# Kernel optimization log

Hardware: AMD Instinct MI355X
Metric: run time of the kernel (lower is better)

The kernel has to match this reference:

```python
import math
import jax, jax.numpy as jnp
import numpy as np

N = 100000
E_RAND = 800000
IN_F, HID, OUT_F, HEADS = 128, 64, 64, 4
NOISE_SCALE = 1.0 * math.sqrt(2.0 * math.log(1.25 / 0.05))  # dp_rate=1, eps=1, del=0.05


def setup_inputs() -> dict:
    key = jax.random.key(0)
    ks = jax.random.split(key, 12)
    x = jax.random.normal(ks[0], (N, IN_F), dtype=jnp.float32)
    src_r = jax.random.randint(ks[1], (E_RAND,), 0, N, dtype=jnp.int32)
    dst_r = jax.random.randint(ks[2], (E_RAND,), 0, N, dtype=jnp.int32)
    loops = jnp.arange(N, dtype=jnp.int32)  # add_self_loop
    src = jnp.concatenate([src_r, loops])
    dst = jnp.concatenate([dst_r, loops])
    # layer 0: GATConv(in=128, out=64, heads=4)
    s0 = 1.0 / math.sqrt(IN_F)
    W0 = jax.random.normal(ks[3], (IN_F, HEADS * HID), dtype=jnp.float32) * s0
    al0 = jax.random.normal(ks[4], (HEADS, HID), dtype=jnp.float32) * 0.1
    ar0 = jax.random.normal(ks[5], (HEADS, HID), dtype=jnp.float32) * 0.1
    b0 = jnp.zeros((HEADS * HID,), dtype=jnp.float32)
    # layer 1: GATConv(in=256, out=64, heads=1)
    s1 = 1.0 / math.sqrt(HEADS * HID)
    W1 = jax.random.normal(ks[6], (HEADS * HID, OUT_F), dtype=jnp.float32) * s1
    al1 = jax.random.normal(ks[7], (1, OUT_F), dtype=jnp.float32) * 0.1
    ar1 = jax.random.normal(ks[8], (1, OUT_F), dtype=jnp.float32) * 0.1
    b1 = jnp.zeros((OUT_F,), dtype=jnp.float32)
    # DP gaussian noise added after first GAT layer (torch.normal(0,1,x.shape))
    noise = jax.random.normal(ks[9], (N, HEADS * HID), dtype=jnp.float32)
    return {"x": x, "src": src, "dst": dst, "W0": W0, "al0": al0, "ar0": ar0,
            "b0": b0, "W1": W1, "al1": al1, "ar1": ar1, "b1": b1, "noise": noise}


def gat_conv(x, src, dst, W, al, ar, b, apply_act):
    """DGL GATConv: per-edge attention, edge softmax over dst, scatter-sum."""
    H, D = al.shape
    h = (x @ W).reshape(-1, H, D)                      # [N,H,D]
    el = jnp.sum(h * al, axis=-1)                      # [N,H]
    er = jnp.sum(h * ar, axis=-1)                      # [N,H]
    e = jax.nn.leaky_relu(el[src] + er[dst], 0.2)      # [E,H]
    emax = jax.ops.segment_max(e, dst, num_segments=N) # [N,H]
    a = jnp.exp(e - emax[dst])
    denom = jax.ops.segment_sum(a, dst, num_segments=N)
    alpha = a / denom[dst]                             # [E,H] edge softmax
    msg = h[src] * alpha[:, :, None]                   # [E,H,D]
    out = jax.ops.segment_sum(msg, dst, num_segments=N) + b.reshape(1, H, D)
    if apply_act:
        out = jax.nn.leaky_relu(out, 0.01)             # F.leaky_relu default slope
    return out.reshape(-1, H * D)                      # flatten(1)


def reference(x, src, dst, W0, al0, ar0, b0, W1, al1, ar1, b1, noise):
    h = gat_conv(x, src, dst, W0, al0, ar0, b0, apply_act=True)   # [N, 256]
    h = h + NOISE_SCALE * noise                                   # DP noise after layer 0
    out = gat_conv(h, src, dst, W1, al1, ar1, b1, apply_act=False)  # [N, 64]
    return out
```

## Files before the change

kernel.cpp:

```cpp
#include <hip/hip_runtime.h>
#include <hip/hip_bf16.h>
#include <math.h>

#define IN_F 128
#define HID 64
#define HEADS 4
#define HD0 (HEADS * HID)
#define OUT_F 64
#define NOISE_SCALE 2.5372725354060904f

typedef __bf16 bf16x8 __attribute__((ext_vector_type(8)));
typedef float f32x4 __attribute__((ext_vector_type(4)));
typedef float f4 __attribute__((ext_vector_type(4)));
typedef unsigned int u4 __attribute__((ext_vector_type(4)));

__device__ __forceinline__ float bf2f(unsigned short u) {
    return __uint_as_float(((unsigned)u) << 16);
}
__device__ __forceinline__ unsigned short f2bf(float f) {
    unsigned u = __float_as_uint(f);
    u = u + 0x7fffu + ((u >> 16) & 1u);
    return (unsigned short)(u >> 16);
}

__device__ __forceinline__ void acc8(float* acc, const uint4& u, float wt) {
    acc[0] += wt * __uint_as_float(u.x << 16);
    acc[1] += wt * __uint_as_float(u.x & 0xffff0000u);
    acc[2] += wt * __uint_as_float(u.y << 16);
    acc[3] += wt * __uint_as_float(u.y & 0xffff0000u);
    acc[4] += wt * __uint_as_float(u.z << 16);
    acc[5] += wt * __uint_as_float(u.z & 0xffff0000u);
    acc[6] += wt * __uint_as_float(u.w << 16);
    acc[7] += wt * __uint_as_float(u.w & 0xffff0000u);
}

__device__ __forceinline__ uint4 pack8(const float4& a, const float4& b) {
    uint4 r;
    r.x = (unsigned)f2bf(a.x) | ((unsigned)f2bf(a.y) << 16);
    r.y = (unsigned)f2bf(a.z) | ((unsigned)f2bf(a.w) << 16);
    r.z = (unsigned)f2bf(b.x) | ((unsigned)f2bf(b.y) << 16);
    r.w = (unsigned)f2bf(b.z) | ((unsigned)f2bf(b.w) << 16);
    return r;
}

__global__ __launch_bounds__(256) void prep_kernel(
    int* __restrict__ deg, int N,
    const float* __restrict__ W0, unsigned short* __restrict__ W0t,
    const float* __restrict__ W1, unsigned short* __restrict__ W1t) {
    const int b = blockIdx.x;
    int i = b * 256 + threadIdx.x;
    if (i < N) deg[i] = 0;
    if (b < (IN_F * HD0) / 256) {
        int n = i / IN_F, k = i % IN_F;
        W0t[i] = f2bf(W0[(size_t)k * HD0 + n]);
    } else if (b < (IN_F * HD0) / 256 + (HD0 * OUT_F) / 256) {
        int j = i - IN_F * HD0;
        int n = j / HD0, k = j % HD0;
        W1t[j] = f2bf(W1[(size_t)k * OUT_F + n]);
    }
}

template <int K, int H, int NT, bool CVT>
__global__ __launch_bounds__(256) void gemm_fused_kernel(
    const void* __restrict__ Asrc, const unsigned short* __restrict__ Bt,
    unsigned short* __restrict__ C, const float* __restrict__ al,
    const float* __restrict__ ar, float* __restrict__ el,
    float* __restrict__ er, int M, int NC) {
    constexpr int BSTR = K + 8;
    constexpr int ASTR = 40;
    constexpr int NROWS = 64 * NT;
    constexpr int CSTR = NROWS + 8;
    __shared__ __align__(16) unsigned short Bs[NROWS * BSTR];
    __shared__ __align__(16) unsigned short As[128 * ASTR];
    const unsigned short* Ab = (const unsigned short*)Asrc;
    const float* Af = (const float*)Asrc;
    const int tid = threadIdx.x;
    const int lane = tid & 63, w = tid >> 6;
    const int row0 = blockIdx.y * 128;
    const int n0 = blockIdx.x * NROWS;
    for (int i = tid; i < NROWS * (K / 8); i += 256) {
        int n = i / (K / 8), kc = i % (K / 8);
        *(uint4*)(Bs + n * BSTR + kc * 8) =
            *(const uint4*)(Bt + (size_t)(n0 + n) * K + kc * 8);
    }
    f32x4 acc[2][4 * NT] = {};
    const int q = lane >> 4, c = lane & 15;
    const int r_st = tid >> 1, hh = tid & 1;
    for (int k0 = 0; k0 < K; k0 += 32) {
        int gr = row0 + r_st;
        uint4 av0 = make_uint4(0, 0, 0, 0), av1 = make_uint4(0, 0, 0, 0);
        if (gr < M) {
            if (CVT) {
                const float* xp = Af + (size_t)gr * K + k0 + hh * 16;
                const float4 fa = *(const float4*)xp;
                const float4 fb = *(const float4*)(xp + 4);
                const float4 fc = *(const float4*)(xp + 8);
                const float4 fd = *(const float4*)(xp + 12);
                av0 = pack8(fa, fb);
                av1 = pack8(fc, fd);
            } else {
                const unsigned short* ap = Ab + (size_t)gr * K + k0 + hh * 16;
                av0 = *(const uint4*)(ap);
                av1 = *(const uint4*)(ap + 8);
            }
        }
        __syncthreads();
        *(uint4*)(As + r_st * ASTR + hh * 16) = av0;
        *(uint4*)(As + r_st * ASTR + hh * 16 + 8) = av1;
        __syncthreads();
        bf16x8 af[2], bfr[4 * NT];
        af[0] = *(const bf16x8*)(As + (w * 32 + c) * ASTR + q * 8);
        af[1] = *(const bf16x8*)(As + (w * 32 + 16 + c) * ASTR + q * 8);
#pragma unroll
        for (int nt = 0; nt < 4 * NT; ++nt)
            bfr[nt] = *(const bf16x8*)(Bs + (nt * 16 + c) * BSTR + k0 + q * 8);
#pragma unroll
        for (int mt = 0; mt < 2; ++mt)
#pragma unroll
            for (int nt = 0; nt < 4 * NT; ++nt)
                acc[mt][nt] = __builtin_amdgcn_mfma_f32_16x16x32_bf16(
                    af[mt], bfr[nt], acc[mt][nt], 0, 0, 0);
    }
    float alv[4 * NT], arv[4 * NT];
#pragma unroll
    for (int nt = 0; nt < 4 * NT; ++nt) {
        alv[nt] = al[n0 + nt * 16 + c];
        arv[nt] = ar[n0 + nt * 16 + c];
    }
    __syncthreads();
    unsigned short* Cs = Bs;
    const int headbase = n0 >> 6;
#pragma unroll
    for (int mt = 0; mt < 2; ++mt) {
#pragma unroll
        for (int r = 0; r < 4; ++r) {
            const int row = w * 32 + mt * 16 + q * 4 + r;
            const int grow = row0 + row;
            const bool ok = grow < M;
#pragma unroll
            for (int g = 0; g < NT; ++g) {
                float elp = 0.f, erp = 0.f;
#pragma unroll
                for (int t = 0; t < 4; ++t) {
                    int nt = g * 4 + t;
                    float v = acc[mt][nt][r];
                    elp += v * alv[nt];
                    erp += v * arv[nt];
                    Cs[row * CSTR + nt * 16 + c] = f2bf(v);
                }
#pragma unroll
                for (int o = 8; o > 0; o >>= 1) {
                    elp += __shfl_down(elp, o, 16);
                    erp += __shfl_down(erp, o, 16);
                }
                if (c == 0 && ok) {
                    el[(size_t)grow * H + headbase + g] = elp;
                    er[(size_t)grow * H + headbase + g] = erp;
                }
            }
        }
    }
    __syncthreads();
    constexpr int CPR = NROWS / 8;
    for (int i = tid; i < 128 * CPR; i += 256) {
        int row = i / CPR, ch = i % CPR;
        int grow = row0 + row;
        if (grow < M)
            *(uint4*)(C + (size_t)grow * NC + n0 + ch * 8) =
                *(const uint4*)(Cs + row * CSTR + ch * 8);
    }
}

__global__ __launch_bounds__(256) void degree_kernel(
    const int* __restrict__ dst, int* __restrict__ deg, int E) {
    int e = blockIdx.x * 256 + threadIdx.x;
    if (e < E) atomicAdd(&deg[dst[e]], 1);
}

__global__ __launch_bounds__(256) void scan_block_kernel(
    const int* __restrict__ deg, int* __restrict__ off,
    int* __restrict__ bsum, int N) {
    __shared__ int s[256];
    int i = blockIdx.x * 256 + threadIdx.x;
    int v = (i < N) ? deg[i] : 0;
    s[threadIdx.x] = v;
    __syncthreads();
    for (int d = 1; d < 256; d <<= 1) {
        int t = (threadIdx.x >= d) ? s[threadIdx.x - d] : 0;
        __syncthreads();
        s[threadIdx.x] += t;
        __syncthreads();
    }
    if (i < N) off[i] = s[threadIdx.x] - v;
    if (threadIdx.x == 255) bsum[blockIdx.x] = s[255];
}

__global__ __launch_bounds__(512) void scan_partials_kernel(int* __restrict__ bsum, int nb) {
    __shared__ int s[512];
    int v = (threadIdx.x < nb) ? bsum[threadIdx.x] : 0;
    s[threadIdx.x] = v;
    __syncthreads();
    for (int d = 1; d < 512; d <<= 1) {
        int t = (threadIdx.x >= d) ? s[threadIdx.x - d] : 0;
        __syncthreads();
        s[threadIdx.x] += t;
        __syncthreads();
    }
    if (threadIdx.x < nb) bsum[threadIdx.x] = s[threadIdx.x] - v;
}

__global__ __launch_bounds__(256) void add_offsets_kernel(
    int* __restrict__ off, int* __restrict__ cur,
    const int* __restrict__ bsum, int N, int E) {
    int i = blockIdx.x * 256 + threadIdx.x;
    if (i < N) {
        int v = off[i] + bsum[blockIdx.x];
        off[i] = v;
        cur[i] = v;
    }
    if (i == 0) off[N] = E;
}

__global__ __launch_bounds__(256) void fill_csr_kernel(
    const int* __restrict__ src, const int* __restrict__ dst,
    int* __restrict__ cur, int* __restrict__ csr_src, int E) {
    int e = blockIdx.x * 256 + threadIdx.x;
    if (e >= E) return;
    int d = dst[e];
    int pos = atomicAdd(&cur[d], 1);
    csr_src[pos] = src[e];
}

__global__ __launch_bounds__(256) void agg0_kernel(
    const int* __restrict__ off, const int* __restrict__ csr_src,
    const unsigned short* __restrict__ h,
    const float* __restrict__ el,
    const float* __restrict__ er,
    const float* __restrict__ b0, const float* __restrict__ noise,
    unsigned short* __restrict__ out, int N) {
    int gt = blockIdx.x * 256 + threadIdx.x;
    int n = gt >> 5;
    if (n >= N) return;
    const int lane = gt & 31;
    const int hd = lane >> 3;
    const int f0 = lane << 3;
    const float ern = er[(size_t)n * 4 + hd];
    const int beg = off[n];
    const int last = off[n + 1] - 1;
    float acc[8] = {0.f, 0.f, 0.f, 0.f, 0.f, 0.f, 0.f, 0.f};
    float l = 0.f;
    for (int p = beg; p <= last; p += 4) {
        int i1 = p + 1, i2 = p + 2, i3 = p + 3;
        const bool v1 = i1 <= last, v2 = i2 <= last, v3 = i3 <= last;
        i1 = v1 ? i1 : last;
        i2 = v2 ? i2 : last;
        i3 = v3 ? i3 : last;
        const int s0 = csr_src[p],  s1 = csr_src[i1];
        const int s2 = csr_src[i2], s3 = csr_src[i3];
        float e0 = el[(size_t)s0 * 4 + hd] + ern;
        float e1 = el[(size_t)s1 * 4 + hd] + ern;
        float e2 = el[(size_t)s2 * 4 + hd] + ern;
        float e3 = el[(size_t)s3 * 4 + hd] + ern;
        const uint4 u0 = *(const uint4*)(h + (size_t)s0 * HD0 + f0);
        const uint4 u1 = *(const uint4*)(h + (size_t)s1 * HD0 + f0);
        const uint4 u2 = *(const uint4*)(h + (size_t)s2 * HD0 + f0);
        const uint4 u3 = *(const uint4*)(h + (size_t)s3 * HD0 + f0);
        e0 = e0 > 0.f ? e0 : 0.2f * e0;
        e1 = e1 > 0.f ? e1 : 0.2f * e1;
        e2 = e2 > 0.f ? e2 : 0.2f * e2;
        e3 = e3 > 0.f ? e3 : 0.2f * e3;
        const float w0 = __expf(e0);
        const float w1 = v1 ? __expf(e1) : 0.f;
        const float w2 = v2 ? __expf(e2) : 0.f;
        const float w3 = v3 ? __expf(e3) : 0.f;
        acc8(acc, u0, w0);
        acc8(acc, u1, w1);
        acc8(acc, u2, w2);
        acc8(acc, u3, w3);
        l += (w0 + w1) + (w2 + w3);
    }
    const float rd = 1.f / l;
    const float4 ba = *(const float4*)(b0 + f0);
    const float4 bb = *(const float4*)(b0 + f0 + 4);
    const f4 na = __builtin_nontemporal_load((const f4*)(noise + (size_t)n * HD0 + f0));
    const f4 nb = __builtin_nontemporal_load((const f4*)(noise + (size_t)n * HD0 + f0 + 4));
    float o[8];
    o[0] = acc[0] * rd + ba.x;
    o[1] = acc[1] * rd + ba.y;
    o[2] = acc[2] * rd + ba.z;
    o[3] = acc[3] * rd + ba.w;
    o[4] = acc[4] * rd + bb.x;
    o[5] = acc[5] * rd + bb.y;
    o[6] = acc[6] * rd + bb.z;
    o[7] = acc[7] * rd + bb.w;
#pragma unroll
    for (int j = 0; j < 8; ++j) o[j] = o[j] > 0.f ? o[j] : 0.01f * o[j];
    o[0] += NOISE_SCALE * na.x;
    o[1] += NOISE_SCALE * na.y;
    o[2] += NOISE_SCALE * na.z;
    o[3] += NOISE_SCALE * na.w;
    o[4] += NOISE_SCALE * nb.x;
    o[5] += NOISE_SCALE * nb.y;
    o[6] += NOISE_SCALE * nb.z;
    o[7] += NOISE_SCALE * nb.w;
    uint4 ov;
    ov.x = (unsigned)f2bf(o[0]) | ((unsigned)f2bf(o[1]) << 16);
    ov.y = (unsigned)f2bf(o[2]) | ((unsigned)f2bf(o[3]) << 16);
    ov.z = (unsigned)f2bf(o[4]) | ((unsigned)f2bf(o[5]) << 16);
    ov.w = (unsigned)f2bf(o[6]) | ((unsigned)f2bf(o[7]) << 16);
    *(uint4*)(out + (size_t)n * HD0 + f0) = ov;
}

__global__ __launch_bounds__(256) void agg1_kernel(
    const int* __restrict__ off, const int* __restrict__ csr_src,
    const unsigned short* __restrict__ h,
    const float* __restrict__ el,
    const float* __restrict__ er,
    const float* __restrict__ b1, float* __restrict__ out, int N) {
    int gt = blockIdx.x * 256 + threadIdx.x;
    int n = gt >> 4;
    if (n >= N) return;
    const int lane = gt & 15;
    const int f0 = lane << 2;
    const float ern = er[n];
    const int beg = off[n];
    const int last = off[n + 1] - 1;
    float a0 = 0.f, a1 = 0.f, a2 = 0.f, a3 = 0.f, l = 0.f;
    for (int p = beg; p <= last; p += 4) {
        int i1 = p + 1, i2 = p + 2, i3 = p + 3;
        const bool v1 = i1 <= last, v2 = i2 <= last, v3 = i3 <= last;
        i1 = v1 ? i1 : last;
        i2 = v2 ? i2 : last;
        i3 = v3 ? i3 : last;
        const int s0 = csr_src[p],  s1 = csr_src[i1];
        const int s2 = csr_src[i2], s3 = csr_src[i3];
        float e0 = el[s0] + ern;
        float e1 = el[s1] + ern;
        float e2 = el[s2] + ern;
        float e3 = el[s3] + ern;
        const ushort4 u0 = *(const ushort4*)(h + (size_t)s0 * 64 + f0);
        const ushort4 u1 = *(const ushort4*)(h + (size_t)s1 * 64 + f0);
        const ushort4 u2 = *(const ushort4*)(h + (size_t)s2 * 64 + f0);
        const ushort4 u3 = *(const ushort4*)(h + (size_t)s3 * 64 + f0);
        e0 = e0 > 0.f ? e0 : 0.2f * e0;
        e1 = e1 > 0.f ? e1 : 0.2f * e1;
        e2 = e2 > 0.f ? e2 : 0.2f * e2;
        e3 = e3 > 0.f ? e3 : 0.2f * e3;
        const float w0 = __expf(e0);
        const float w1 = v1 ? __expf(e1) : 0.f;
        const float w2 = v2 ? __expf(e2) : 0.f;
        const float w3 = v3 ? __expf(e3) : 0.f;
        a0 += w0 * bf2f(u0.x) + w1 * bf2f(u1.x) + w2 * bf2f(u2.x) + w3 * bf2f(u3.x);
        a1 += w0 * bf2f(u0.y) + w1 * bf2f(u1.y) + w2 * bf2f(u2.y) + w3 * bf2f(u3.y);
        a2 += w0 * bf2f(u0.z) + w1 * bf2f(u1.z) + w2 * bf2f(u2.z) + w3 * bf2f(u3.z);
        a3 += w0 * bf2f(u0.w) + w1 * bf2f(u1.w) + w2 * bf2f(u2.w) + w3 * bf2f(u3.w);
        l += (w0 + w1) + (w2 + w3);
    }
    const float rd = 1.f / l;
    const float4 bv = *(const float4*)(b1 + f0);
    float4 o;
    o.x = a0 * rd + bv.x;
    o.y = a1 * rd + bv.y;
    o.z = a2 * rd + bv.z;
    o.w = a3 * rd + bv.w;
    *(float4*)(out + (size_t)n * 64 + f0) = o;
}

extern "C" void kernel_launch(void* const* d_in, const int* in_sizes, int n_in,
                              void* d_out, int out_size, void* d_ws, size_t ws_size,
                              hipStream_t stream) {
    const float* x     = (const float*)d_in[0];
    const int*   src   = (const int*)d_in[1];
    const int*   dst   = (const int*)d_in[2];
    const float* W0    = (const float*)d_in[3];
    const float* al0   = (const float*)d_in[4];
    const float* ar0   = (const float*)d_in[5];
    const float* b0    = (const float*)d_in[6];
    const float* W1    = (const float*)d_in[7];
    const float* al1   = (const float*)d_in[8];
    const float* ar1   = (const float*)d_in[9];
    const float* b1    = (const float*)d_in[10];
    const float* noise = (const float*)d_in[11];

    const int N = in_sizes[0] / IN_F;
    const int E = in_sizes[1];
    const int NB = (N + 255) / 256;

    char* p = (char*)d_ws;
    unsigned short* h0     = (unsigned short*)p; p += (size_t)N * HD0 * 2;
    unsigned short* agg0b  = (unsigned short*)p; p += (size_t)N * HD0 * 2;
    unsigned short* h1     = (unsigned short*)p; p += (size_t)N * OUT_F * 2;
    unsigned short* W0t    = (unsigned short*)p; p += (size_t)IN_F * HD0 * 2;
    unsigned short* W1t    = (unsigned short*)p; p += (size_t)HD0 * OUT_F * 2;
    float* el     = (float*)p; p += (size_t)N * HEADS * 4;
    float* er     = (float*)p; p += (size_t)N * HEADS * 4;
    int* deg    = (int*)p; p += (size_t)N * 4;
    int* cur    = (int*)p; p += (size_t)N * 4;
    int* off    = (int*)p; p += ((size_t)N + 4) * 4;
    int* bsum   = (int*)p; p += 512 * 4;
    int* csr_src= (int*)p; p += (size_t)E * 4;

    prep_kernel<<<NB, 256, 0, stream>>>(deg, N, W0, W0t, W1, W1t);

    degree_kernel<<<(E + 255) / 256, 256, 0, stream>>>(dst, deg, E);
    scan_block_kernel<<<NB, 256, 0, stream>>>(deg, off, bsum, N);
    scan_partials_kernel<<<1, 512, 0, stream>>>(bsum, NB);
    add_offsets_kernel<<<NB, 256, 0, stream>>>(off, cur, bsum, N, E);
    fill_csr_kernel<<<(E + 255) / 256, 256, 0, stream>>>(src, dst, cur, csr_src, E);

    const int MB = (N + 127) / 128;

    {
        dim3 grid(HD0 / 128, MB);
        gemm_fused_kernel<IN_F, HEADS, 2, true><<<grid, 256, 0, stream>>>(
            (const void*)x, W0t, h0, al0, ar0, el, er, N, HD0);
    }
    agg0_kernel<<<(unsigned)(((size_t)N * 32 + 255) / 256), 256, 0, stream>>>(
        off, csr_src, h0, el, er, b0, noise, agg0b, N);

    {
        dim3 grid(OUT_F / 64, MB);
        gemm_fused_kernel<HD0, 1, 1, false><<<grid, 256, 0, stream>>>(
            (const void*)agg0b, W1t, h1, al1, ar1, el, er, N, OUT_F);
    }
    agg1_kernel<<<(unsigned)(((size_t)N * 16 + 255) / 256), 256, 0, stream>>>(
        off, csr_src, h1, el, er, b1, (float*)d_out, N);
}
```

Before: 431.4 us.

## Fuse CSR build kernels into one cooperative kernel with grid syncs

Replaces the six separate preprocessing launches (weight transpose, degree count, block scan, partial scan, offset add, CSR fill) with a single cooperative kernel of 1024 blocks that uses grid-wide syncs between phases. The aim is to cut per-launch overhead and the idle gaps between small kernels. In exchange it adds grid barrier costs and fewer concurrent blocks for the atomic-heavy phases. The cooperative launch's return value is not checked, so an oversized grid would fail silently.

```diff
diff --git a/kernel.cpp b/kernel.cpp
--- a/kernel.cpp
+++ b/kernel.cpp
@@ -1,6 +1,9 @@
 #include <hip/hip_runtime.h>
 #include <hip/hip_bf16.h>
+#include <hip/hip_cooperative_groups.h>
 #include <math.h>
+
+namespace cg = cooperative_groups;
 
 #define IN_F 128
 #define HID 64
@@ -43,20 +46,74 @@
     return r;
 }
 
-__global__ __launch_bounds__(256) void prep_kernel(
-    int* __restrict__ deg, int N,
+__global__ __launch_bounds__(256) void build_kernel(
+    const int* __restrict__ src, const int* __restrict__ dst,
+    int* __restrict__ deg, int* __restrict__ off, int* __restrict__ cur,
+    int* __restrict__ tsum, int* __restrict__ csr_src, int N, int E, int ntiles,
     const float* __restrict__ W0, unsigned short* __restrict__ W0t,
     const float* __restrict__ W1, unsigned short* __restrict__ W1t) {
-    const int b = blockIdx.x;
-    int i = b * 256 + threadIdx.x;
-    if (i < N) deg[i] = 0;
-    if (b < (IN_F * HD0) / 256) {
+    cg::grid_group grid = cg::this_grid();
+    __shared__ int s[256];
+    __shared__ int s2[256];
+    const int tid = threadIdx.x;
+    const int gsize = gridDim.x * 256;
+    const int gtid = blockIdx.x * 256 + tid;
+    for (int i = gtid; i < N; i += gsize) deg[i] = 0;
+    for (int i = gtid; i < IN_F * HD0; i += gsize) {
         int n = i / IN_F, k = i % IN_F;
         W0t[i] = f2bf(W0[(size_t)k * HD0 + n]);
-    } else if (b < (IN_F * HD0) / 256 + (HD0 * OUT_F) / 256) {
-        int j = i - IN_F * HD0;
-        int n = j / HD0, k = j % HD0;
-        W1t[j] = f2bf(W1[(size_t)k * OUT_F + n]);
+    }
+    for (int i = gtid; i < HD0 * OUT_F; i += gsize) {
+        int n = i / HD0, k = i % HD0;
+        W1t[i] = f2bf(W1[(size_t)k * OUT_F + n]);
+    }
+    grid.sync();
+    for (int e = gtid; e < E; e += gsize) atomicAdd(&deg[dst[e]], 1);
+    grid.sync();
+    for (int t = blockIdx.x; t < ntiles; t += gridDim.x) {
+        int i = t * 256 + tid;
+        int v = (i < N) ? deg[i] : 0;
+        s[tid] = v;
+        __syncthreads();
+        for (int d = 1; d < 256; d <<= 1) {
+            int tt = (tid >= d) ? s[tid - d] : 0;
+            __syncthreads();
+            s[tid] += tt;
+            __syncthreads();
+        }
+        if (i < N) off[i] = s[tid] - v;
+        if (tid == 255) tsum[t] = s[255];
+        __syncthreads();
+    }
+    grid.sync();
+    if (blockIdx.x == 0) {
+        int a = (2 * tid < ntiles) ? tsum[2 * tid] : 0;
+        int b = (2 * tid + 1 < ntiles) ? tsum[2 * tid + 1] : 0;
+        int pair = a + b;
+        s2[tid] = pair;
+        __syncthreads();
+        for (int d = 1; d < 256; d <<= 1) {
+            int tt = (tid >= d) ? s2[tid - d] : 0;
+            __syncthreads();
+            s2[tid] += tt;
+            __syncthreads();
+        }
+        int excl = s2[tid] - pair;
+        if (2 * tid < ntiles) tsum[2 * tid] = excl;
+        if (2 * tid + 1 < ntiles) tsum[2 * tid + 1] = excl + a;
+    }
+    grid.sync();
+    for (int i = gtid; i < N; i += gsize) {
+        int v = off[i] + tsum[i >> 8];
+        off[i] = v;
+        cur[i] = v;
+    }
+    if (gtid == 0) off[N] = E;
+    grid.sync();
+    for (int e = gtid; e < E; e += gsize) {
+        int d = dst[e];
+        int pos = atomicAdd(&cur[d], 1);
+        csr_src[pos] = src[e];
     }
 }
 
@@ -169,66 +226,6 @@
             *(uint4*)(C + (size_t)grow * NC + n0 + ch * 8) =
                 *(const uint4*)(Cs + row * CSTR + ch * 8);
     }
-}
-
-__global__ __launch_bounds__(256) void degree_kernel(
-    const int* __restrict__ dst, int* __restrict__ deg, int E) {
-    int e = blockIdx.x * 256 + threadIdx.x;
-    if (e < E) atomicAdd(&deg[dst[e]], 1);
-}
-
-__global__ __launch_bounds__(256) void scan_block_kernel(
-    const int* __restrict__ deg, int* __restrict__ off,
-    int* __restrict__ bsum, int N) {
-    __shared__ int s[256];
-    int i = blockIdx.x * 256 + threadIdx.x;
-    int v = (i < N) ? deg[i] : 0;
-    s[threadIdx.x] = v;
-    __syncthreads();
-    for (int d = 1; d < 256; d <<= 1) {
-        int t = (threadIdx.x >= d) ? s[threadIdx.x - d] : 0;
-        __syncthreads();
-        s[threadIdx.x] += t;
-        __syncthreads();
-    }
-    if (i < N) off[i] = s[threadIdx.x] - v;
-    if (threadIdx.x == 255) bsum[blockIdx.x] = s[255];
-}
-
-__global__ __launch_bounds__(512) void scan_partials_kernel(int* __restrict__ bsum, int nb) {
-    __shared__ int s[512];
-    int v = (threadIdx.x < nb) ? bsum[threadIdx.x] : 0;
-    s[threadIdx.x] = v;
-    __syncthreads();
-    for (int d = 1; d < 512; d <<= 1) {
-        int t = (threadIdx.x >= d) ? s[threadIdx.x - d] : 0;
-        __syncthreads();
-        s[threadIdx.x] += t;
-        __syncthreads();
-    }
-    if (threadIdx.x < nb) bsum[threadIdx.x] = s[threadIdx.x] - v;
-}
-
-__global__ __launch_bounds__(256) void add_offsets_kernel(
-    int* __restrict__ off, int* __restrict__ cur,
-    const int* __restrict__ bsum, int N, int E) {
-    int i = blockIdx.x * 256 + threadIdx.x;
-    if (i < N) {
-        int v = off[i] + bsum[blockIdx.x];
-        off[i] = v;
-        cur[i] = v;
-    }
-    if (i == 0) off[N] = E;
-}
-
-__global__ __launch_bounds__(256) void fill_csr_kernel(
-    const int* __restrict__ src, const int* __restrict__ dst,
-    int* __restrict__ cur, int* __restrict__ csr_src, int E) {
-    int e = blockIdx.x * 256 + threadIdx.x;
-    if (e >= E) return;
-    int d = dst[e];
-    int pos = atomicAdd(&cur[d], 1);
-    csr_src[pos] = src[e];
 }
 
 __global__ __launch_bounds__(256) void agg0_kernel(
@@ -397,16 +394,18 @@
     int* deg    = (int*)p; p += (size_t)N * 4;
     int* cur    = (int*)p; p += (size_t)N * 4;
     int* off    = (int*)p; p += ((size_t)N + 4) * 4;
-    int* bsum   = (int*)p; p += 512 * 4;
+    int* tsum   = (int*)p; p += 512 * 4;
     int* csr_src= (int*)p; p += (size_t)E * 4;
 
-    prep_kernel<<<NB, 256, 0, stream>>>(deg, N, W0, W0t, W1, W1t);
-
-    degree_kernel<<<(E + 255) / 256, 256, 0, stream>>>(dst, deg, E);
-    scan_block_kernel<<<NB, 256, 0, stream>>>(deg, off, bsum, N);
-    scan_partials_kernel<<<1, 512, 0, stream>>>(bsum, NB);
-    add_offsets_kernel<<<NB, 256, 0, stream>>>(off, cur, bsum, N, E);
-    fill_csr_kernel<<<(E + 255) / 256, 256, 0, stream>>>(src, dst, cur, csr_src, E);
+    {
+        int ntiles = NB;
+        void* args[] = {
+            (void*)&src, (void*)&dst, (void*)&deg, (void*)&off, (void*)&cur,
+            (void*)&tsum, (void*)&csr_src, (void*)&N, (void*)&E, (void*)&ntiles,
+            (void*)&W0, (void*)&W0t, (void*)&W1, (void*)&W1t};
+        hipLaunchCooperativeKernel((const void*)build_kernel, dim3(1024), dim3(256),
+                                   args, 0, stream);
+    }
 
     const int MB = (N + 127) / 128;
 
```

Result: slower. 927.0 us (+114.9%).

## Fuse three-pass offset scan into single-pass decoupled look-back scan

Applied to the files above, without the earlier changes.

Replaces the block-scan, partial-scan and add-offsets kernels with one kernel that uses a decoupled look-back across blocks through flag-tagged 64-bit words in global memory. The combo flags are zeroed in the existing prep kernel. This removes two kernel launches and their dependent round trips. In exchange it relies on earlier blocks being scheduled before later ones spin-wait, and the look-back is serial in thread 0.

```diff
diff --git a/kernel.cpp b/kernel.cpp
--- a/kernel.cpp
+++ b/kernel.cpp
@@ -45,11 +45,13 @@
 
 __global__ __launch_bounds__(256) void prep_kernel(
     int* __restrict__ deg, int N,
+    unsigned long long* __restrict__ combo, int ntiles,
     const float* __restrict__ W0, unsigned short* __restrict__ W0t,
     const float* __restrict__ W1, unsigned short* __restrict__ W1t) {
     const int b = blockIdx.x;
     int i = b * 256 + threadIdx.x;
     if (i < N) deg[i] = 0;
+    if (i < ntiles) combo[i] = 0ULL;
     if (b < (IN_F * HD0) / 256) {
         int n = i / IN_F, k = i % IN_F;
         W0t[i] = f2bf(W0[(size_t)k * HD0 + n]);
@@ -177,46 +179,51 @@
     if (e < E) atomicAdd(&deg[dst[e]], 1);
 }
 
-__global__ __launch_bounds__(256) void scan_block_kernel(
-    const int* __restrict__ deg, int* __restrict__ off,
-    int* __restrict__ bsum, int N) {
+__global__ __launch_bounds__(256) void scan_fused_kernel(
+    const int* __restrict__ deg, int* __restrict__ off, int* __restrict__ cur,
+    unsigned long long* __restrict__ combo, int N, int E) {
+    const int t = blockIdx.x;
     __shared__ int s[256];
-    int i = blockIdx.x * 256 + threadIdx.x;
-    int v = (i < N) ? deg[i] : 0;
-    s[threadIdx.x] = v;
+    __shared__ int sbase;
+    const int tid = threadIdx.x;
+    const int i = t * 256 + tid;
+    const int v = (i < N) ? deg[i] : 0;
+    s[tid] = v;
     __syncthreads();
     for (int d = 1; d < 256; d <<= 1) {
-        int t = (threadIdx.x >= d) ? s[threadIdx.x - d] : 0;
+        int tt = (tid >= d) ? s[tid - d] : 0;
         __syncthreads();
-        s[threadIdx.x] += t;
+        s[tid] += tt;
         __syncthreads();
     }
-    if (i < N) off[i] = s[threadIdx.x] - v;
-    if (threadIdx.x == 255) bsum[blockIdx.x] = s[255];
-}
-
-__global__ __launch_bounds__(512) void scan_partials_kernel(int* __restrict__ bsum, int nb) {
-    __shared__ int s[512];
-    int v = (threadIdx.x < nb) ? bsum[threadIdx.x] : 0;
-    s[threadIdx.x] = v;
+    const int tilesum = s[255];
+    if (tid == 0) {
+        if (t == 0) {
+            atomicExch(&combo[0], (2ULL << 32) | (unsigned)tilesum);
+            sbase = 0;
+        } else {
+            atomicExch(&combo[t], (1ULL << 32) | (unsigned)tilesum);
+            int run = 0;
+            int j = t - 1;
+            while (true) {
+                unsigned long long c;
+                do {
+                    c = atomicAdd(&combo[j], 0ULL);
+                } while ((c >> 32) == 0ULL);
+                run += (int)(c & 0xffffffffULL);
+                if ((c >> 32) == 2ULL) break;
+                --j;
+            }
+            sbase = run;
+            atomicExch(&combo[t], (2ULL << 32) | (unsigned)(run + tilesum));
+        }
+    }
     __syncthreads();
-    for (int d = 1; d < 512; d <<= 1) {
-        int t = (threadIdx.x >= d) ? s[threadIdx.x - d] : 0;
-        __syncthreads();
-        s[threadIdx.x] += t;
-        __syncthreads();
-    }
-    if (threadIdx.x < nb) bsum[threadIdx.x] = s[threadIdx.x] - v;
-}
-
-__global__ __launch_bounds__(256) void add_offsets_kernel(
-    int* __restrict__ off, int* __restrict__ cur,
-    const int* __restrict__ bsum, int N, int E) {
-    int i = blockIdx.x * 256 + threadIdx.x;
+    const int base = sbase;
     if (i < N) {
-        int v = off[i] + bsum[blockIdx.x];
-        off[i] = v;
-        cur[i] = v;
+        int o = base + s[tid] - v;
+        off[i] = o;
+        cur[i] = o;
     }
     if (i == 0) off[N] = E;
 }
@@ -397,15 +404,13 @@
     int* deg    = (int*)p; p += (size_t)N * 4;
     int* cur    = (int*)p; p += (size_t)N * 4;
     int* off    = (int*)p; p += ((size_t)N + 4) * 4;
-    int* bsum   = (int*)p; p += 512 * 4;
+    unsigned long long* combo = (unsigned long long*)p; p += 512 * 8;
     int* csr_src= (int*)p; p += (size_t)E * 4;
 
-    prep_kernel<<<NB, 256, 0, stream>>>(deg, N, W0, W0t, W1, W1t);
+    prep_kernel<<<NB, 256, 0, stream>>>(deg, N, combo, NB, W0, W0t, W1, W1t);
 
     degree_kernel<<<(E + 255) / 256, 256, 0, stream>>>(dst, deg, E);
-    scan_block_kernel<<<NB, 256, 0, stream>>>(deg, off, bsum, N);
-    scan_partials_kernel<<<1, 512, 0, stream>>>(bsum, NB);
-    add_offsets_kernel<<<NB, 256, 0, stream>>>(off, cur, bsum, N, E);
+    scan_fused_kernel<<<NB, 256, 0, stream>>>(deg, off, cur, combo, N, E);
     fill_csr_kernel<<<(E + 255) / 256, 256, 0, stream>>>(src, dst, cur, csr_src, E);
 
     const int MB = (N + 127) / 128;
```

Measured after the change: 435.3 us. No clear change (+0.9%).
